# Performance work log

Measured on AMD Instinct MI355X. Metric: run time of the kernel, lower is better.

Reference implementation:

```python
import jax, jax.numpy as jnp
import numpy as np

B, S, HID = 1, 2048, 4096
H, HKV, DFULL, D = 32, 8, 128, 96
GROUPS = H // HKV
SCALE = DFULL ** -0.5  # scaling uses the FULL head_dim per the source
ROPE_THETA = 10000.0


def setup_inputs() -> dict:
    key = jax.random.key(0)
    ks = jax.random.split(key, 8)
    hidden_states = jax.random.normal(ks[0], (B, S, HID), jnp.float32)
    # standard HF Llama RoPE tables over the FULL head dim
    inv_freq = 1.0 / (ROPE_THETA ** (jnp.arange(0, DFULL, 2, dtype=jnp.float32) / DFULL))
    ang = jnp.arange(S, dtype=jnp.float32)[:, None] * inv_freq[None, :]  # [S, DFULL/2]
    emb = jnp.concatenate([ang, ang], axis=-1)  # [S, DFULL]
    cos = jnp.cos(emb)[None]  # [1, S, DFULL]
    sin = jnp.sin(emb)[None]
    # per-kv-head frequency indices: lo half in [0, DFULL/2), hi half = lo + DFULL/2
    half, dh = DFULL // 2, D // 2
    idx_lo = jax.random.randint(ks[1], (HKV, dh), 0, half)
    indices = jnp.concatenate([idx_lo, idx_lo + half], axis=-1).astype(jnp.int32)  # [HKV, D]
    s = 0.02
    Wq = jax.random.normal(ks[2], (H * D, HID), jnp.float32) * s
    Wk = jax.random.normal(ks[3], (HKV * D, HID), jnp.float32) * s
    Wv = jax.random.normal(ks[4], (HKV * D, HID), jnp.float32) * s
    Wo = jax.random.normal(ks[5], (HID, H * D), jnp.float32) * s
    return {"hidden_states": hidden_states, "cos": cos, "sin": sin,
            "indices": indices, "Wq": Wq, "Wk": Wk, "Wv": Wv, "Wo": Wo}


def rotate_half(x):
    x1, x2 = jnp.split(x, 2, axis=-1)
    return jnp.concatenate([-x2, x1], axis=-1)


def reference(hidden_states, cos, sin, indices, Wq, Wk, Wv, Wo):
    b, s, _ = hidden_states.shape
    # QKV projections (no bias), reshape to [B, heads, S, D]
    q = (hidden_states @ Wq.T).reshape(b, s, H, D).transpose(0, 2, 1, 3)
    k = (hidden_states @ Wk.T).reshape(b, s, HKV, D).transpose(0, 2, 1, 3)
    v = (hidden_states @ Wv.T).reshape(b, s, HKV, D).transpose(0, 2, 1, 3)
    # indexed RoPE: gather per-kv-head frequencies from the full-dim tables
    cos_h = cos[:, :, indices].transpose(0, 2, 1, 3)  # [B, HKV, S, D]
    sin_h = sin[:, :, indices].transpose(0, 2, 1, 3)
    cos_q = jnp.repeat(cos_h, GROUPS, axis=1)  # [B, H, S, D]
    sin_q = jnp.repeat(sin_h, GROUPS, axis=1)
    q = q * cos_q + rotate_half(q) * sin_q
    k = k * cos_h + rotate_half(k) * sin_h
    # GQA: repeat kv to num_attention_heads
    k = jnp.repeat(k, GROUPS, axis=1)  # [B, H, S, D]
    v = jnp.repeat(v, GROUPS, axis=1)
    scores = jnp.einsum('bhqd,bhkd->bhqk', q, k) * SCALE
    causal = jnp.tril(jnp.ones((s, s), dtype=bool))
    scores = jnp.where(causal[None, None], scores, jnp.finfo(scores.dtype).min)
    probs = jax.nn.softmax(scores, axis=-1)
    out = jnp.einsum('bhqk,bhkd->bhqd', probs, v)  # [B, H, S, D]
    out = out.transpose(0, 2, 1, 3).reshape(b, s, H * D)
    return out @ Wo.T
```

## Files before the change

kernel.cpp:

```cpp
#include <hip/hip_runtime.h>

typedef unsigned short u16;
typedef unsigned int u32;
typedef __bf16 bf16x8 __attribute__((ext_vector_type(8)));
typedef float f32x4 __attribute__((ext_vector_type(4)));

#define SCALE_Q2 0.12751743443398106f

#define GLDS16(gp, lp)                                                        \
  __builtin_amdgcn_global_load_lds(                                           \
      (const __attribute__((address_space(1))) void*)(gp),                    \
      (__attribute__((address_space(3))) void*)(lp), 16, 0, 0)

__device__ __forceinline__ u16 f2bf(float f) {
  u32 u = __builtin_bit_cast(u32, f);
  u += 0x7fffu + ((u >> 16) & 1u);
  return (u16)(u >> 16);
}
__device__ __forceinline__ float bf2f(u16 b) {
  u32 u = ((u32)b) << 16;
  return __builtin_bit_cast(float, u);
}

__global__ __launch_bounds__(256) void cvt_all(const float* __restrict__ hs,
                                               const float* __restrict__ Wq,
                                               const float* __restrict__ Wk,
                                               const float* __restrict__ Wv,
                                               const float* __restrict__ Wo,
                                               u16* __restrict__ hsB,
                                               u16* __restrict__ wqkvB,
                                               u16* __restrict__ woB) {
  u32 b = blockIdx.x;
  const float* src;
  u16* dst;
  u32 i;
  if (b < 8192u) {
    src = hs; dst = hsB; i = b * 256u + threadIdx.x;
  } else if (b < 20480u) {
    src = Wq; dst = wqkvB; i = (b - 8192u) * 256u + threadIdx.x;
  } else if (b < 23552u) {
    src = Wk; dst = wqkvB + 3072u * 4096u; i = (b - 20480u) * 256u + threadIdx.x;
  } else if (b < 26624u) {
    src = Wv; dst = wqkvB + 3840u * 4096u; i = (b - 23552u) * 256u + threadIdx.x;
  } else {
    src = Wo; dst = woB; i = (b - 26624u) * 256u + threadIdx.x;
  }
  float4 v = ((const float4*)src)[i];
  u32 lo = (u32)f2bf(v.x) | ((u32)f2bf(v.y) << 16);
  u32 hi = (u32)f2bf(v.z) | ((u32)f2bf(v.w) << 16);
  ((uint2*)dst)[i] = make_uint2(lo, hi);
}

template <int NREP, bool BF16OUT>
__global__ __launch_bounds__(512, 2) void gemm8p(const u16* __restrict__ A,
                                                 const u16* __restrict__ B,
                                                 void* __restrict__ Cout,
                                                 int M, int N, int K) {
  constexpr int BN = NREP * 64;
  __shared__ u16 As[2 * 256 * 64];
  __shared__ u16 Bs[2 * BN * 64];
  const int tid = threadIdx.x;
  const int w = tid >> 6, lane = tid & 63, quad = lane >> 4, c16 = lane & 15;

  const int nx = gridDim.x;
  const int orig = blockIdx.y * nx + blockIdx.x;
  const int nwg = nx * gridDim.y;
  const int id = (orig & 7) * (nwg >> 3) + (orig >> 3);
  const int n0 = (id % nx) * BN, m0 = (id / nx) * 256;

  const int wm = (w & 1) * 128, wn = (w >> 1) * (NREP * 16);
  const int srow8 = lane >> 3, scg = (lane & 7) ^ srow8;
  const u16* Ag = A + (size_t)(m0 + w * 8 + srow8) * K + scg * 8;
  const u16* Bg = B + (size_t)(n0 + w * 8 + srow8) * K + scg * 8;
  const int axor = c16 & 7;

  f32x4 acc[8][NREP];
#pragma unroll
  for (int i = 0; i < 8; ++i)
#pragma unroll
    for (int j = 0; j < NREP; ++j) acc[i][j] = (f32x4){0.f, 0.f, 0.f, 0.f};

  const int NT = K >> 6;

#pragma unroll
  for (int j = 0; j < 4; ++j)
    GLDS16(Ag + (size_t)(j * 64) * K, &As[(j * 64 + w * 8) * 64]);
#pragma unroll
  for (int j = 0; j < NREP; ++j)
    GLDS16(Bg + (size_t)(j * 64) * K, &Bs[(j * 64 + w * 8) * 64]);

  for (int t = 0; t < NT; ++t) {
    const int sl = t & 1;
    const u16* as = &As[sl * (256 * 64)];
    const u16* bs = &Bs[sl * (BN * 64)];
    u16* asn = &As[(sl ^ 1) * (256 * 64)];
    u16* bsn = &Bs[(sl ^ 1) * (BN * 64)];
    const int kn = (t + 1) * 64;
    const bool pf = (t + 1 < NT);

    if (pf) {
#pragma unroll
      for (int j = 0; j < 4; ++j)
        GLDS16(Ag + (size_t)(j * 64) * K + kn, &asn[(j * 64 + w * 8) * 64]);
      asm volatile("s_waitcnt vmcnt(4)" ::: "memory");
    } else {
      asm volatile("s_waitcnt vmcnt(0)" ::: "memory");
    }
    __builtin_amdgcn_s_barrier();
    asm volatile("" ::: "memory");

    bf16x8 bfr[NREP][2];
#pragma unroll
    for (int nt = 0; nt < NREP; ++nt)
#pragma unroll
      for (int kk = 0; kk < 2; ++kk)
        bfr[nt][kk] = *(const bf16x8*)&bs[(wn + nt * 16 + c16) * 64 +
                                          (((kk * 4 + quad) ^ axor) * 8)];

#pragma unroll
    for (int ph = 0; ph < 4; ++ph) {
      bf16x8 afr[2][2];
#pragma unroll
      for (int i = 0; i < 2; ++i)
#pragma unroll
        for (int kk = 0; kk < 2; ++kk)
          afr[i][kk] = *(const bf16x8*)&as[(wm + (ph * 2 + i) * 16 + c16) * 64 +
                                            (((kk * 4 + quad) ^ axor) * 8)];
      if (ph == 1 && pf) {
#pragma unroll
        for (int j = 0; j < NREP; ++j)
          GLDS16(Bg + (size_t)(j * 64) * K + kn, &bsn[(j * 64 + w * 8) * 64]);
      }
      __builtin_amdgcn_s_setprio(1);
#pragma unroll
      for (int i = 0; i < 2; ++i)
#pragma unroll
        for (int nt = 0; nt < NREP; ++nt)
#pragma unroll
          for (int kk = 0; kk < 2; ++kk)
            acc[ph * 2 + i][nt] = __builtin_amdgcn_mfma_f32_16x16x32_bf16(
                afr[i][kk], bfr[nt][kk], acc[ph * 2 + i][nt], 0, 0, 0);
      __builtin_amdgcn_s_setprio(0);
    }
    asm volatile("" ::: "memory");
    __builtin_amdgcn_s_barrier();
  }

#pragma unroll
  for (int mt = 0; mt < 8; ++mt)
#pragma unroll
    for (int nt = 0; nt < NREP; ++nt)
#pragma unroll
      for (int r = 0; r < 4; ++r) {
        int m = m0 + wm + mt * 16 + quad * 4 + r;
        int n = n0 + wn + nt * 16 + c16;
        if (BF16OUT)
          ((u16*)Cout)[(size_t)m * N + n] = f2bf(acc[mt][nt][r]);
        else
          ((float*)Cout)[(size_t)m * N + n] = acc[mt][nt][r];
      }
}

__global__ __launch_bounds__(256) void rope_vt(const u16* __restrict__ qkv,
                                               const float* __restrict__ cosb,
                                               const float* __restrict__ sinb,
                                               const int* __restrict__ idxs,
                                               u16* __restrict__ qB,
                                               u16* __restrict__ kB,
                                               u16* __restrict__ vtB) {
  __shared__ u16 T[64 * 34];
  u32 bid = blockIdx.x;
  if (bid < 30720u) {
    u32 i = bid * 256u + threadIdx.x;
    const u32 NQ = 2048u * 32u * 96u;
    if (i < NQ) {
      u32 s = i / 3072u, rem = i % 3072u;
      u32 h = rem / 96u, d = rem % 96u;
      u32 hkv = h >> 2;
      u32 base = s * 4608u + h * 96u + d;
      float x = bf2f(qkv[base]);
      float pv = (d < 48u) ? -bf2f(qkv[base + 48u]) : bf2f(qkv[base - 48u]);
      int idx = idxs[hkv * 96u + d];
      float c = cosb[s * 128u + idx], sn = sinb[s * 128u + idx];
      qB[(h * 2048u + s) * 96u + d] = f2bf((x * c + pv * sn) * SCALE_Q2);
    } else {
      u32 j = i - NQ;
      u32 s = j / 768u, rem = j % 768u;
      u32 hkv = rem / 96u, d = rem % 96u;
      u32 base = s * 4608u + 3072u + hkv * 96u + d;
      float x = bf2f(qkv[base]);
      float pv = (d < 48u) ? -bf2f(qkv[base + 48u]) : bf2f(qkv[base - 48u]);
      int idx = idxs[hkv * 96u + d];
      float c = cosb[s * 128u + idx], sn = sinb[s * 128u + idx];
      kB[(hkv * 2048u + s) * 96u + d] = f2bf(x * c + pv * sn);
    }
  } else {
    u32 b2 = bid - 30720u;
    const int s0 = (b2 & 31) * 64, d0 = (int)(b2 >> 5) * 32;
    const int tx = threadIdx.x & 31, ty = threadIdx.x >> 5;
#pragma unroll
    for (int it = 0; it < 8; it++) {
      int row = it * 8 + ty;
      T[row * 34 + tx] = qkv[(size_t)(s0 + row) * 4608 + 3840 + d0 + tx];
    }
    __syncthreads();
    const int sx = threadIdx.x & 63, dy = threadIdx.x >> 6;
#pragma unroll
    for (int it = 0; it < 8; it++) {
      int d = it * 4 + dy;
      vtB[(size_t)(d0 + d) * 2048 + s0 + sx] = T[sx * 34 + d];
    }
  }
}

__global__ __launch_bounds__(256) void attn_kernel(const u16* __restrict__ qB,
                                                   const u16* __restrict__ kB,
                                                   const u16* __restrict__ vtB,
                                                   u16* __restrict__ aoB) {
  __shared__ u16 Ks[2][64 * 96];
  __shared__ u16 Vs[2][96 * 64];
  __shared__ u16 Ps[4 * 16 * 64];
  const int tid = threadIdx.x;
  const int w = tid >> 6, lane = tid & 63, quad = lane >> 4, c16 = lane & 15;
  const u32 id = blockIdx.x;
  const int hkv = id & 7;
  const int h = 4 * hkv + ((id >> 3) & 3);
  const int pr = id >> 5;
  u16* pw = Ps + w * (16 * 64);

  size_t voff[3];
#pragma unroll
  for (int it = 0; it < 3; it++) {
    int j = it * 256 + tid;
    int row = j >> 3, c = (j & 7) ^ (row & 7);
    voff[it] = (size_t)row * 2048 + c * 8;
  }
  const u16* kbase = kB + (size_t)hkv * 2048 * 96;
  const u16* vbase = vtB + (size_t)hkv * 96 * 2048;

  auto stage = [&](int buf, int kt) {
    const int k0 = kt * 64;
#pragma unroll
    for (int it = 0; it < 3; it++) {
      GLDS16(kbase + (size_t)k0 * 96 + (it * 256 + tid) * 8,
             &Ks[buf][(it * 256 + w * 64) * 8]);
      GLDS16(vbase + voff[it] + k0, &Vs[buf][(it * 256 + w * 64) * 8]);
    }
  };

  bf16x8 vones;
#pragma unroll
  for (int i = 0; i < 8; i++) vones[i] = (__bf16)1.0f;

  for (int ph = 0; ph < 2; ph++) {
    const int qt = ph ? (31 - pr) : pr;
    const int m_base = qt * 64 + w * 16;

    bf16x8 qf[3];
    {
      const u16* qrow = qB + ((size_t)h * 2048 + m_base + c16) * 96;
#pragma unroll
      for (int t = 0; t < 3; t++) qf[t] = *(const bf16x8*)(qrow + t * 32 + quad * 8);
    }
    f32x4 o[6], ol;
#pragma unroll
    for (int dt = 0; dt < 6; dt++) o[dt] = (f32x4){0.f, 0.f, 0.f, 0.f};
    ol = (f32x4){0.f, 0.f, 0.f, 0.f};

    stage(0, 0);
    __syncthreads();

    for (int kt = 0; kt <= qt; kt++) {
      const int cur = kt & 1;
      if (kt < qt) stage(cur ^ 1, kt + 1);

      f32x4 sacc[4];
#pragma unroll
      for (int nt = 0; nt < 4; nt++) sacc[nt] = (f32x4){0.f, 0.f, 0.f, 0.f};
      __builtin_amdgcn_s_setprio(1);
#pragma unroll
      for (int nt = 0; nt < 4; nt++)
#pragma unroll
        for (int t = 0; t < 3; t++) {
          bf16x8 kf = *(const bf16x8*)(&Ks[cur][(nt * 16 + c16) * 96 + t * 32 + quad * 8]);
          sacc[nt] = __builtin_amdgcn_mfma_f32_16x16x32_bf16(qf[t], kf, sacc[nt], 0, 0, 0);
        }
      __builtin_amdgcn_s_setprio(0);

      const int k0 = kt * 64;
      if (kt == qt) {
#pragma unroll
        for (int r = 0; r < 4; r++) {
          int row_abs = m_base + quad * 4 + r;
#pragma unroll
          for (int nt = 0; nt < 4; nt++)
            if (k0 + nt * 16 + c16 > row_abs) sacc[nt][r] = -__builtin_inff();
        }
      }

#pragma unroll
      for (int r = 0; r < 4; r++) {
        int mrow = quad * 4 + r, m7 = mrow & 7;
#pragma unroll
        for (int nt = 0; nt < 4; nt++) {
          float p = __builtin_amdgcn_exp2f(sacc[nt][r]);
          int chunk = (nt * 2 + (c16 >> 3)) ^ m7;
          pw[mrow * 64 + chunk * 8 + (c16 & 7)] =
              (u16)(__builtin_bit_cast(u32, p) >> 16);
        }
      }
      bf16x8 pf[2];
#pragma unroll
      for (int kti = 0; kti < 2; kti++) {
        int chunk = (kti * 4 + quad) ^ (c16 & 7);
        pf[kti] = *(const bf16x8*)(&pw[c16 * 64 + chunk * 8]);
      }
      __builtin_amdgcn_s_setprio(1);
#pragma unroll
      for (int kti = 0; kti < 2; kti++) {
        ol = __builtin_amdgcn_mfma_f32_16x16x32_bf16(pf[kti], vones, ol, 0, 0, 0);
#pragma unroll
        for (int dt = 0; dt < 6; dt++) {
          int row = dt * 16 + c16;
          int vch = (kti * 4 + quad) ^ (row & 7);
          bf16x8 vf = *(const bf16x8*)(&Vs[cur][row * 64 + vch * 8]);
          o[dt] = __builtin_amdgcn_mfma_f32_16x16x32_bf16(pf[kti], vf, o[dt], 0, 0, 0);
        }
      }
      __builtin_amdgcn_s_setprio(0);

      __syncthreads();
    }

#pragma unroll
    for (int r = 0; r < 4; r++) {
      float inv = 1.0f / ol[r];
      int row = m_base + quad * 4 + r;
#pragma unroll
      for (int dt = 0; dt < 6; dt++)
        aoB[(size_t)row * 3072 + h * 96 + dt * 16 + c16] = f2bf(o[dt][r] * inv);
    }
  }
}

extern "C" void kernel_launch(void* const* d_in, const int* in_sizes, int n_in,
                              void* d_out, int out_size, void* d_ws, size_t ws_size,
                              hipStream_t stream) {
  const float* hs   = (const float*)d_in[0];
  const float* cosb = (const float*)d_in[1];
  const float* sinb = (const float*)d_in[2];
  const int*   idxs = (const int*)d_in[3];
  const float* Wq   = (const float*)d_in[4];
  const float* Wk   = (const float*)d_in[5];
  const float* Wv   = (const float*)d_in[6];
  const float* Wo   = (const float*)d_in[7];
  float* out = (float*)d_out;
  char* ws = (char*)d_ws;

  u16* hsB   = (u16*)(ws);
  u16* wqkvB = (u16*)(ws + 16777216);
  u16* woB   = (u16*)(ws + 54525952);
  u16* qkvB  = (u16*)(ws + 79691776);
  u16* qB    = (u16*)(ws + 98566144);
  u16* kB    = (u16*)(ws + 111149056);
  u16* vtB   = (u16*)(ws + 114294784);
  u16* aoB   = (u16*)(ws + 117440512);

  cvt_all<<<38912, 256, 0, stream>>>(hs, Wq, Wk, Wv, Wo, hsB, wqkvB, woB);

  gemm8p<3, true><<<dim3(24, 8), 512, 0, stream>>>(hsB, wqkvB, qkvB, 2048, 4608, 4096);

  rope_vt<<<31488, 256, 0, stream>>>(qkvB, cosb, sinb, idxs, qB, kB, vtB);

  attn_kernel<<<512, 256, 0, stream>>>(qB, kB, vtB, aoB);

  gemm8p<2, false><<<dim3(32, 8), 512, 0, stream>>>(aoB, woB, out, 2048, 4096, 3072);
}
```

Baseline: 421.0 us.

## Restructure GEMM main loop into four barrier-separated phases with split prefetch

Rewrites the bf16 GEMM inner loop into four phases, each split by k-half and m-half. Each phase loads its LDS fragments, passes a barrier, then issues MFMAs. The global-to-LDS prefetch of the next tile is spread across the phases in pieces (A halves and B) with finer vmcnt waits. The goal is to overlap memory traffic with MFMA work and smooth out issue contention. In exchange it adds more barriers per k-tile, which could add synchronisation stalls.

```diff
diff --git a/kernel.cpp b/kernel.cpp
--- a/kernel.cpp
+++ b/kernel.cpp
@@ -11,6 +11,19 @@
   __builtin_amdgcn_global_load_lds(                                           \
       (const __attribute__((address_space(1))) void*)(gp),                    \
       (__attribute__((address_space(3))) void*)(lp), 16, 0, 0)
+
+#define BARRIER()                                                             \
+  do {                                                                        \
+    asm volatile("" ::: "memory");                                            \
+    __builtin_amdgcn_s_barrier();                                             \
+    asm volatile("" ::: "memory");                                            \
+  } while (0)
+
+template <int N>
+__device__ __forceinline__ void vmwait() {
+  if constexpr (N == 0) asm volatile("s_waitcnt vmcnt(0)" ::: "memory");
+  else if constexpr (N == 2) asm volatile("s_waitcnt vmcnt(2)" ::: "memory");
+}
 
 __device__ __forceinline__ u16 f2bf(float f) {
   u32 u = __builtin_bit_cast(u32, f);
@@ -52,7 +65,7 @@
 }
 
 template <int NREP, bool BF16OUT>
-__global__ __launch_bounds__(512, 2) void gemm8p(const u16* __restrict__ A,
+__global__ __launch_bounds__(512, 2) void gemm4p(const u16* __restrict__ A,
                                                  const u16* __restrict__ B,
                                                  void* __restrict__ Cout,
                                                  int M, int N, int K) {
@@ -82,69 +95,83 @@
 
   const int NT = K >> 6;
 
-#pragma unroll
-  for (int j = 0; j < 4; ++j)
-    GLDS16(Ag + (size_t)(j * 64) * K, &As[(j * 64 + w * 8) * 64]);
-#pragma unroll
-  for (int j = 0; j < NREP; ++j)
-    GLDS16(Bg + (size_t)(j * 64) * K, &Bs[(j * 64 + w * 8) * 64]);
+#define STAGE_A(t, j)                                                         \
+  GLDS16(Ag + (size_t)((j) * 64) * K + (size_t)(t) * 64,                      \
+         &As[((t) & 1) * (256 * 64) + ((j) * 64 + w * 8) * 64])
+#define STAGE_B(t, j)                                                         \
+  GLDS16(Bg + (size_t)((j) * 64) * K + (size_t)(t) * 64,                      \
+         &Bs[((t) & 1) * (BN * 64) + ((j) * 64 + w * 8) * 64])
+
+  STAGE_A(0, 0);
+  STAGE_A(0, 2);
+#pragma unroll
+  for (int j = 0; j < NREP; ++j) STAGE_B(0, j);
+  STAGE_A(0, 1);
+  STAGE_A(0, 3);
+  vmwait<2>();
+  BARRIER();
 
   for (int t = 0; t < NT; ++t) {
-    const int sl = t & 1;
-    const u16* as = &As[sl * (256 * 64)];
-    const u16* bs = &Bs[sl * (BN * 64)];
-    u16* asn = &As[(sl ^ 1) * (256 * 64)];
-    u16* bsn = &Bs[(sl ^ 1) * (BN * 64)];
-    const int kn = (t + 1) * 64;
+    const u16* as = &As[(t & 1) * (256 * 64)];
+    const u16* bs = &Bs[(t & 1) * (BN * 64)];
     const bool pf = (t + 1 < NT);
+    bf16x8 af[4], bf[NREP];
+
+    auto lda = [&](int mh, int kk) {
+#pragma unroll
+      for (int mt = 0; mt < 4; ++mt)
+        af[mt] = *(const bf16x8*)&as[(wm + (mh * 4 + mt) * 16 + c16) * 64 +
+                                     (((kk * 4 + quad) ^ axor) * 8)];
+    };
+    auto ldb = [&](int kk) {
+#pragma unroll
+      for (int nt = 0; nt < NREP; ++nt)
+        bf[nt] = *(const bf16x8*)&bs[(wn + nt * 16 + c16) * 64 +
+                                     (((kk * 4 + quad) ^ axor) * 8)];
+    };
+    auto mma = [&](int mh) {
+      __builtin_amdgcn_s_setprio(1);
+#pragma unroll
+      for (int mt = 0; mt < 4; ++mt)
+#pragma unroll
+        for (int nt = 0; nt < NREP; ++nt)
+          acc[mh * 4 + mt][nt] = __builtin_amdgcn_mfma_f32_16x16x32_bf16(
+              af[mt], bf[nt], acc[mh * 4 + mt][nt], 0, 0, 0);
+      __builtin_amdgcn_s_setprio(0);
+    };
+
+    if (pf) { STAGE_A(t + 1, 0); STAGE_A(t + 1, 2); }
+    lda(0, 0);
+    ldb(0);
+    BARRIER();
+    mma(0);
+    if (pf) vmwait<2>(); else vmwait<0>();
+    BARRIER();
 
     if (pf) {
 #pragma unroll
-      for (int j = 0; j < 4; ++j)
-        GLDS16(Ag + (size_t)(j * 64) * K + kn, &asn[(j * 64 + w * 8) * 64]);
-      asm volatile("s_waitcnt vmcnt(4)" ::: "memory");
-    } else {
-      asm volatile("s_waitcnt vmcnt(0)" ::: "memory");
-    }
-    __builtin_amdgcn_s_barrier();
-    asm volatile("" ::: "memory");
-
-    bf16x8 bfr[NREP][2];
-#pragma unroll
-    for (int nt = 0; nt < NREP; ++nt)
-#pragma unroll
-      for (int kk = 0; kk < 2; ++kk)
-        bfr[nt][kk] = *(const bf16x8*)&bs[(wn + nt * 16 + c16) * 64 +
-                                          (((kk * 4 + quad) ^ axor) * 8)];
-
-#pragma unroll
-    for (int ph = 0; ph < 4; ++ph) {
-      bf16x8 afr[2][2];
-#pragma unroll
-      for (int i = 0; i < 2; ++i)
-#pragma unroll
-        for (int kk = 0; kk < 2; ++kk)
-          afr[i][kk] = *(const bf16x8*)&as[(wm + (ph * 2 + i) * 16 + c16) * 64 +
-                                            (((kk * 4 + quad) ^ axor) * 8)];
-      if (ph == 1 && pf) {
-#pragma unroll
-        for (int j = 0; j < NREP; ++j)
-          GLDS16(Bg + (size_t)(j * 64) * K + kn, &bsn[(j * 64 + w * 8) * 64]);
-      }
-      __builtin_amdgcn_s_setprio(1);
-#pragma unroll
-      for (int i = 0; i < 2; ++i)
-#pragma unroll
-        for (int nt = 0; nt < NREP; ++nt)
-#pragma unroll
-          for (int kk = 0; kk < 2; ++kk)
-            acc[ph * 2 + i][nt] = __builtin_amdgcn_mfma_f32_16x16x32_bf16(
-                afr[i][kk], bfr[nt][kk], acc[ph * 2 + i][nt], 0, 0, 0);
-      __builtin_amdgcn_s_setprio(0);
-    }
-    asm volatile("" ::: "memory");
-    __builtin_amdgcn_s_barrier();
+      for (int j = 0; j < NREP; ++j) STAGE_B(t + 1, j);
+    }
+    lda(1, 0);
+    BARRIER();
+    mma(1);
+    BARRIER();
+
+    if (pf) { STAGE_A(t + 1, 1); STAGE_A(t + 1, 3); }
+    lda(0, 1);
+    ldb(1);
+    BARRIER();
+    mma(0);
+    BARRIER();
+
+    lda(1, 1);
+    BARRIER();
+    mma(1);
+    if (pf) vmwait<2>();
+    BARRIER();
   }
+#undef STAGE_A
+#undef STAGE_B
 
 #pragma unroll
   for (int mt = 0; mt < 8; ++mt)
@@ -368,11 +395,11 @@
 
   cvt_all<<<38912, 256, 0, stream>>>(hs, Wq, Wk, Wv, Wo, hsB, wqkvB, woB);
 
-  gemm8p<3, true><<<dim3(24, 8), 512, 0, stream>>>(hsB, wqkvB, qkvB, 2048, 4608, 4096);
+  gemm4p<3, true><<<dim3(24, 8), 512, 0, stream>>>(hsB, wqkvB, qkvB, 2048, 4608, 4096);
 
   rope_vt<<<31488, 256, 0, stream>>>(qkvB, cosb, sinb, idxs, qB, kB, vtB);
 
   attn_kernel<<<512, 256, 0, stream>>>(qB, kB, vtB, aoB);
 
-  gemm8p<2, false><<<dim3(32, 8), 512, 0, stream>>>(aoB, woB, out, 2048, 4096, 3072);
-}
+  gemm4p<2, false><<<dim3(32, 8), 512, 0, stream>>>(aoB, woB, out, 2048, 4096, 3072);
+}
```

Result: slower. 498.2 us (+18.3%).

## Fuse V transpose into QKV GEMM epilogue and widen attention query tiles

Applied to the files above, without the earlier changes.

The QKV GEMM epilogue now writes V columns straight into the transposed vtB layout, so the separate transpose blocks in the rope kernel are removed. The attention kernel doubles each wave's query rows to 32, so every K/V tile staged in LDS feeds twice as many MFMAs. Because of that, the grid is halved to 256 blocks. The attention loop also replaces __syncthreads with explicit vmcnt waits and barriers. The cost is more registers per wave and fewer blocks to fill the GPU, which risks occupancy and load balance.

```diff
diff --git a/kernel.cpp b/kernel.cpp
--- a/kernel.cpp
+++ b/kernel.cpp
@@ -11,6 +11,20 @@
   __builtin_amdgcn_global_load_lds(                                           \
       (const __attribute__((address_space(1))) void*)(gp),                    \
       (__attribute__((address_space(3))) void*)(lp), 16, 0, 0)
+
+#define BARRIER()                                                             \
+  do {                                                                        \
+    asm volatile("" ::: "memory");                                            \
+    __builtin_amdgcn_s_barrier();                                             \
+    asm volatile("" ::: "memory");                                            \
+  } while (0)
+
+template <int N>
+__device__ __forceinline__ void vmwait() {
+  if constexpr (N == 0) asm volatile("s_waitcnt vmcnt(0)" ::: "memory");
+  else if constexpr (N == 4) asm volatile("s_waitcnt vmcnt(4)" ::: "memory");
+  else if constexpr (N == 6) asm volatile("s_waitcnt vmcnt(6)" ::: "memory");
+}
 
 __device__ __forceinline__ u16 f2bf(float f) {
   u32 u = __builtin_bit_cast(u32, f);
@@ -55,6 +69,7 @@
 __global__ __launch_bounds__(512, 2) void gemm8p(const u16* __restrict__ A,
                                                  const u16* __restrict__ B,
                                                  void* __restrict__ Cout,
+                                                 u16* __restrict__ vtB, int nv,
                                                  int M, int N, int K) {
   constexpr int BN = NREP * 64;
   __shared__ u16 As[2 * 256 * 64];
@@ -102,9 +117,9 @@
 #pragma unroll
       for (int j = 0; j < 4; ++j)
         GLDS16(Ag + (size_t)(j * 64) * K + kn, &asn[(j * 64 + w * 8) * 64]);
-      asm volatile("s_waitcnt vmcnt(4)" ::: "memory");
+      vmwait<4>();
     } else {
-      asm volatile("s_waitcnt vmcnt(0)" ::: "memory");
+      vmwait<0>();
     }
     __builtin_amdgcn_s_barrier();
     asm volatile("" ::: "memory");
@@ -146,70 +161,62 @@
     __builtin_amdgcn_s_barrier();
   }
 
-#pragma unroll
-  for (int mt = 0; mt < 8; ++mt)
-#pragma unroll
-    for (int nt = 0; nt < NREP; ++nt)
-#pragma unroll
-      for (int r = 0; r < 4; ++r) {
-        int m = m0 + wm + mt * 16 + quad * 4 + r;
-        int n = n0 + wn + nt * 16 + c16;
-        if (BF16OUT)
-          ((u16*)Cout)[(size_t)m * N + n] = f2bf(acc[mt][nt][r]);
-        else
-          ((float*)Cout)[(size_t)m * N + n] = acc[mt][nt][r];
-      }
-}
-
-__global__ __launch_bounds__(256) void rope_vt(const u16* __restrict__ qkv,
-                                               const float* __restrict__ cosb,
-                                               const float* __restrict__ sinb,
-                                               const int* __restrict__ idxs,
-                                               u16* __restrict__ qB,
-                                               u16* __restrict__ kB,
-                                               u16* __restrict__ vtB) {
-  __shared__ u16 T[64 * 34];
-  u32 bid = blockIdx.x;
-  if (bid < 30720u) {
-    u32 i = bid * 256u + threadIdx.x;
-    const u32 NQ = 2048u * 32u * 96u;
-    if (i < NQ) {
-      u32 s = i / 3072u, rem = i % 3072u;
-      u32 h = rem / 96u, d = rem % 96u;
-      u32 hkv = h >> 2;
-      u32 base = s * 4608u + h * 96u + d;
-      float x = bf2f(qkv[base]);
-      float pv = (d < 48u) ? -bf2f(qkv[base + 48u]) : bf2f(qkv[base - 48u]);
-      int idx = idxs[hkv * 96u + d];
-      float c = cosb[s * 128u + idx], sn = sinb[s * 128u + idx];
-      qB[(h * 2048u + s) * 96u + d] = f2bf((x * c + pv * sn) * SCALE_Q2);
-    } else {
-      u32 j = i - NQ;
-      u32 s = j / 768u, rem = j % 768u;
-      u32 hkv = rem / 96u, d = rem % 96u;
-      u32 base = s * 4608u + 3072u + hkv * 96u + d;
-      float x = bf2f(qkv[base]);
-      float pv = (d < 48u) ? -bf2f(qkv[base + 48u]) : bf2f(qkv[base - 48u]);
-      int idx = idxs[hkv * 96u + d];
-      float c = cosb[s * 128u + idx], sn = sinb[s * 128u + idx];
-      kB[(hkv * 2048u + s) * 96u + d] = f2bf(x * c + pv * sn);
-    }
+  if (BF16OUT && n0 >= nv) {
+#pragma unroll
+    for (int mt = 0; mt < 8; ++mt)
+#pragma unroll
+      for (int nt = 0; nt < NREP; ++nt) {
+        int d_col = n0 - nv + wn + nt * 16 + c16;
+        int s_base = m0 + wm + mt * 16 + quad * 4;
+        u32 lo = (u32)f2bf(acc[mt][nt][0]) | ((u32)f2bf(acc[mt][nt][1]) << 16);
+        u32 hi = (u32)f2bf(acc[mt][nt][2]) | ((u32)f2bf(acc[mt][nt][3]) << 16);
+        *(uint2*)&vtB[(size_t)d_col * 2048 + s_base] = make_uint2(lo, hi);
+      }
   } else {
-    u32 b2 = bid - 30720u;
-    const int s0 = (b2 & 31) * 64, d0 = (int)(b2 >> 5) * 32;
-    const int tx = threadIdx.x & 31, ty = threadIdx.x >> 5;
-#pragma unroll
-    for (int it = 0; it < 8; it++) {
-      int row = it * 8 + ty;
-      T[row * 34 + tx] = qkv[(size_t)(s0 + row) * 4608 + 3840 + d0 + tx];
-    }
-    __syncthreads();
-    const int sx = threadIdx.x & 63, dy = threadIdx.x >> 6;
-#pragma unroll
-    for (int it = 0; it < 8; it++) {
-      int d = it * 4 + dy;
-      vtB[(size_t)(d0 + d) * 2048 + s0 + sx] = T[sx * 34 + d];
-    }
+#pragma unroll
+    for (int mt = 0; mt < 8; ++mt)
+#pragma unroll
+      for (int nt = 0; nt < NREP; ++nt)
+#pragma unroll
+        for (int r = 0; r < 4; ++r) {
+          int m = m0 + wm + mt * 16 + quad * 4 + r;
+          int n = n0 + wn + nt * 16 + c16;
+          if (BF16OUT)
+            ((u16*)Cout)[(size_t)m * N + n] = f2bf(acc[mt][nt][r]);
+          else
+            ((float*)Cout)[(size_t)m * N + n] = acc[mt][nt][r];
+        }
+  }
+}
+
+__global__ __launch_bounds__(256) void rope_kernel(const u16* __restrict__ qkv,
+                                                   const float* __restrict__ cosb,
+                                                   const float* __restrict__ sinb,
+                                                   const int* __restrict__ idxs,
+                                                   u16* __restrict__ qB,
+                                                   u16* __restrict__ kB) {
+  u32 i = blockIdx.x * 256u + threadIdx.x;
+  const u32 NQ = 2048u * 32u * 96u;
+  if (i < NQ) {
+    u32 s = i / 3072u, rem = i % 3072u;
+    u32 h = rem / 96u, d = rem % 96u;
+    u32 hkv = h >> 2;
+    u32 base = s * 4608u + h * 96u + d;
+    float x = bf2f(qkv[base]);
+    float pv = (d < 48u) ? -bf2f(qkv[base + 48u]) : bf2f(qkv[base - 48u]);
+    int idx = idxs[hkv * 96u + d];
+    float c = cosb[s * 128u + idx], sn = sinb[s * 128u + idx];
+    qB[(h * 2048u + s) * 96u + d] = f2bf((x * c + pv * sn) * SCALE_Q2);
+  } else {
+    u32 j = i - NQ;
+    u32 s = j / 768u, rem = j % 768u;
+    u32 hkv = rem / 96u, d = rem % 96u;
+    u32 base = s * 4608u + 3072u + hkv * 96u + d;
+    float x = bf2f(qkv[base]);
+    float pv = (d < 48u) ? -bf2f(qkv[base + 48u]) : bf2f(qkv[base - 48u]);
+    int idx = idxs[hkv * 96u + d];
+    float c = cosb[s * 128u + idx], sn = sinb[s * 128u + idx];
+    kB[(hkv * 2048u + s) * 96u + d] = f2bf(x * c + pv * sn);
   }
 }
 
@@ -219,14 +226,14 @@
                                                    u16* __restrict__ aoB) {
   __shared__ u16 Ks[2][64 * 96];
   __shared__ u16 Vs[2][96 * 64];
-  __shared__ u16 Ps[4 * 16 * 64];
+  __shared__ u16 Ps[4 * 32 * 64];
   const int tid = threadIdx.x;
   const int w = tid >> 6, lane = tid & 63, quad = lane >> 4, c16 = lane & 15;
   const u32 id = blockIdx.x;
   const int hkv = id & 7;
   const int h = 4 * hkv + ((id >> 3) & 3);
   const int pr = id >> 5;
-  u16* pw = Ps + w * (16 * 64);
+  u16* pw = Ps + w * (32 * 64);
 
   size_t voff[3];
 #pragma unroll
@@ -253,93 +260,121 @@
   for (int i = 0; i < 8; i++) vones[i] = (__bf16)1.0f;
 
   for (int ph = 0; ph < 2; ph++) {
-    const int qt = ph ? (31 - pr) : pr;
-    const int m_base = qt * 64 + w * 16;
-
-    bf16x8 qf[3];
-    {
-      const u16* qrow = qB + ((size_t)h * 2048 + m_base + c16) * 96;
-#pragma unroll
-      for (int t = 0; t < 3; t++) qf[t] = *(const bf16x8*)(qrow + t * 32 + quad * 8);
-    }
-    f32x4 o[6], ol;
-#pragma unroll
-    for (int dt = 0; dt < 6; dt++) o[dt] = (f32x4){0.f, 0.f, 0.f, 0.f};
-    ol = (f32x4){0.f, 0.f, 0.f, 0.f};
+    const int qt = ph ? (15 - pr) : pr;
+    const int m_base = qt * 128 + w * 32;
+
+    bf16x8 qf[2][3];
+#pragma unroll
+    for (int mt = 0; mt < 2; mt++) {
+      const u16* qrow = qB + ((size_t)h * 2048 + m_base + mt * 16 + c16) * 96;
+#pragma unroll
+      for (int t = 0; t < 3; t++)
+        qf[mt][t] = *(const bf16x8*)(qrow + t * 32 + quad * 8);
+    }
+    f32x4 o[2][6], ol[2];
+#pragma unroll
+    for (int mt = 0; mt < 2; mt++) {
+#pragma unroll
+      for (int dt = 0; dt < 6; dt++) o[mt][dt] = (f32x4){0.f, 0.f, 0.f, 0.f};
+      ol[mt] = (f32x4){0.f, 0.f, 0.f, 0.f};
+    }
 
     stage(0, 0);
-    __syncthreads();
-
-    for (int kt = 0; kt <= qt; kt++) {
+    const int last = 2 * qt + 1;
+
+    for (int kt = 0; kt <= last; kt++) {
       const int cur = kt & 1;
-      if (kt < qt) stage(cur ^ 1, kt + 1);
-
-      f32x4 sacc[4];
-#pragma unroll
-      for (int nt = 0; nt < 4; nt++) sacc[nt] = (f32x4){0.f, 0.f, 0.f, 0.f};
+      if (kt < last) {
+        stage(cur ^ 1, kt + 1);
+        vmwait<6>();
+      } else {
+        vmwait<0>();
+      }
+      BARRIER();
+
+      f32x4 sacc[2][4];
+#pragma unroll
+      for (int mt = 0; mt < 2; mt++)
+#pragma unroll
+        for (int nt = 0; nt < 4; nt++) sacc[mt][nt] = (f32x4){0.f, 0.f, 0.f, 0.f};
       __builtin_amdgcn_s_setprio(1);
 #pragma unroll
       for (int nt = 0; nt < 4; nt++)
 #pragma unroll
         for (int t = 0; t < 3; t++) {
           bf16x8 kf = *(const bf16x8*)(&Ks[cur][(nt * 16 + c16) * 96 + t * 32 + quad * 8]);
-          sacc[nt] = __builtin_amdgcn_mfma_f32_16x16x32_bf16(qf[t], kf, sacc[nt], 0, 0, 0);
+#pragma unroll
+          for (int mt = 0; mt < 2; mt++)
+            sacc[mt][nt] = __builtin_amdgcn_mfma_f32_16x16x32_bf16(
+                qf[mt][t], kf, sacc[mt][nt], 0, 0, 0);
         }
       __builtin_amdgcn_s_setprio(0);
 
       const int k0 = kt * 64;
-      if (kt == qt) {
+      if (kt >= 2 * qt) {
+#pragma unroll
+        for (int mt = 0; mt < 2; mt++)
+#pragma unroll
+          for (int r = 0; r < 4; r++) {
+            int row_abs = m_base + mt * 16 + quad * 4 + r;
+#pragma unroll
+            for (int nt = 0; nt < 4; nt++)
+              if (k0 + nt * 16 + c16 > row_abs) sacc[mt][nt][r] = -__builtin_inff();
+          }
+      }
+
+#pragma unroll
+      for (int mt = 0; mt < 2; mt++)
 #pragma unroll
         for (int r = 0; r < 4; r++) {
-          int row_abs = m_base + quad * 4 + r;
-#pragma unroll
-          for (int nt = 0; nt < 4; nt++)
-            if (k0 + nt * 16 + c16 > row_abs) sacc[nt][r] = -__builtin_inff();
+          int mrow = mt * 16 + quad * 4 + r, m7 = mrow & 7;
+#pragma unroll
+          for (int nt = 0; nt < 4; nt++) {
+            float p = __builtin_amdgcn_exp2f(sacc[mt][nt][r]);
+            int chunk = (nt * 2 + (c16 >> 3)) ^ m7;
+            pw[mrow * 64 + chunk * 8 + (c16 & 7)] =
+                (u16)(__builtin_bit_cast(u32, p) >> 16);
+          }
         }
-      }
-
-#pragma unroll
-      for (int r = 0; r < 4; r++) {
-        int mrow = quad * 4 + r, m7 = mrow & 7;
-#pragma unroll
-        for (int nt = 0; nt < 4; nt++) {
-          float p = __builtin_amdgcn_exp2f(sacc[nt][r]);
-          int chunk = (nt * 2 + (c16 >> 3)) ^ m7;
-          pw[mrow * 64 + chunk * 8 + (c16 & 7)] =
-              (u16)(__builtin_bit_cast(u32, p) >> 16);
+      bf16x8 pf[2][2];
+#pragma unroll
+      for (int mt = 0; mt < 2; mt++)
+#pragma unroll
+        for (int kti = 0; kti < 2; kti++) {
+          int chunk = (kti * 4 + quad) ^ (c16 & 7);
+          pf[mt][kti] = *(const bf16x8*)(&pw[(mt * 16 + c16) * 64 + chunk * 8]);
         }
-      }
-      bf16x8 pf[2];
+      __builtin_amdgcn_s_setprio(1);
 #pragma unroll
       for (int kti = 0; kti < 2; kti++) {
-        int chunk = (kti * 4 + quad) ^ (c16 & 7);
-        pf[kti] = *(const bf16x8*)(&pw[c16 * 64 + chunk * 8]);
-      }
-      __builtin_amdgcn_s_setprio(1);
-#pragma unroll
-      for (int kti = 0; kti < 2; kti++) {
-        ol = __builtin_amdgcn_mfma_f32_16x16x32_bf16(pf[kti], vones, ol, 0, 0, 0);
+#pragma unroll
+        for (int mt = 0; mt < 2; mt++)
+          ol[mt] = __builtin_amdgcn_mfma_f32_16x16x32_bf16(pf[mt][kti], vones, ol[mt], 0, 0, 0);
 #pragma unroll
         for (int dt = 0; dt < 6; dt++) {
           int row = dt * 16 + c16;
           int vch = (kti * 4 + quad) ^ (row & 7);
           bf16x8 vf = *(const bf16x8*)(&Vs[cur][row * 64 + vch * 8]);
-          o[dt] = __builtin_amdgcn_mfma_f32_16x16x32_bf16(pf[kti], vf, o[dt], 0, 0, 0);
+#pragma unroll
+          for (int mt = 0; mt < 2; mt++)
+            o[mt][dt] = __builtin_amdgcn_mfma_f32_16x16x32_bf16(pf[mt][kti], vf, o[mt][dt], 0, 0, 0);
         }
       }
       __builtin_amdgcn_s_setprio(0);
 
-      __syncthreads();
-    }
-
-#pragma unroll
-    for (int r = 0; r < 4; r++) {
-      float inv = 1.0f / ol[r];
-      int row = m_base + quad * 4 + r;
-#pragma unroll
-      for (int dt = 0; dt < 6; dt++)
-        aoB[(size_t)row * 3072 + h * 96 + dt * 16 + c16] = f2bf(o[dt][r] * inv);
-    }
+      BARRIER();
+    }
+
+#pragma unroll
+    for (int mt = 0; mt < 2; mt++)
+#pragma unroll
+      for (int r = 0; r < 4; r++) {
+        float inv = 1.0f / ol[mt][r];
+        int row = m_base + mt * 16 + quad * 4 + r;
+#pragma unroll
+        for (int dt = 0; dt < 6; dt++)
+          aoB[(size_t)row * 3072 + h * 96 + dt * 16 + c16] = f2bf(o[mt][dt][r] * inv);
+      }
   }
 }
 
@@ -368,11 +403,13 @@
 
   cvt_all<<<38912, 256, 0, stream>>>(hs, Wq, Wk, Wv, Wo, hsB, wqkvB, woB);
 
-  gemm8p<3, true><<<dim3(24, 8), 512, 0, stream>>>(hsB, wqkvB, qkvB, 2048, 4608, 4096);
-
-  rope_vt<<<31488, 256, 0, stream>>>(qkvB, cosb, sinb, idxs, qB, kB, vtB);
-
-  attn_kernel<<<512, 256, 0, stream>>>(qB, kB, vtB, aoB);
-
-  gemm8p<2, false><<<dim3(32, 8), 512, 0, stream>>>(aoB, woB, out, 2048, 4096, 3072);
-}
+  gemm8p<3, true><<<dim3(24, 8), 512, 0, stream>>>(hsB, wqkvB, qkvB, vtB, 3840,
+                                                   2048, 4608, 4096);
+
+  rope_kernel<<<30720, 256, 0, stream>>>(qkvB, cosb, sinb, idxs, qB, kB);
+
+  attn_kernel<<<256, 256, 0, stream>>>(qB, kB, vtB, aoB);
+
+  gemm8p<2, false><<<dim3(32, 8), 512, 0, stream>>>(aoB, woB, out, nullptr, 1 << 30,
+                                                    2048, 4096, 3072);
+}
```

Result: slower. 432.3 us (+2.7%).
